# Optimization experiments

Hardware: AMD Instinct MI355X
Metric: run time of the kernel (lower is better)

The kernel has to match this reference:

```python
import jax, jax.numpy as jnp
import numpy as np

# Loss hyperparameters (from init_kwargs defaults)
ALPHA, BETA, GAMMA = 1.0, 2.0, 1.0
DAY_W, NIGHT_W = 2.0, 0.5
PEAK_WIN_W, PEAK_WIN = 3.0, 2
HIGH_POWER_W, POWER_PCT = 1.5, 0.75
HOURS = 24

B, S = 4096, 4032  # seq_len = 24 * 168 days


def setup_inputs() -> dict:
    key = jax.random.key(0)
    k1, k2 = jax.random.split(key)
    y_true = jax.random.uniform(k1, (B, S), dtype=jnp.float32)
    # predictions = truth + noise, clipped to be realistic power values
    y_pred = y_true + 0.1 * jax.random.normal(k2, (B, S), dtype=jnp.float32)
    return {"y_pred": y_pred, "y_true": y_true}


def _daily_peaks(y, day_mask):
    # y, day_mask: (B, D, H). Peaks restricted to daytime hours.
    masked = jnp.where(day_mask, y, jnp.float32(-1e9))
    times = jnp.argmax(masked, axis=-1)                                   # (B, D) int
    vals = jnp.take_along_axis(y, times[..., None], axis=-1)[..., 0]      # (B, D)
    return times, vals


def reference(y_pred, y_true):
    b, s = y_true.shape
    d = s // HOURS
    # default is_daytime: hour-of-day in [6, 20]
    hour = jnp.arange(HOURS, dtype=jnp.int32)
    day_hour_mask = (hour >= 6) & (hour <= 20)                            # (H,)
    is_daytime = jnp.broadcast_to(day_hour_mask[None, None, :], (b, d, HOURS))

    yt = y_true.reshape(b, d, HOURS)
    yp = y_pred.reshape(b, d, HOURS)

    true_times, true_peaks = _daily_peaks(yt, is_daytime)
    pred_times, pred_peaks = _daily_peaks(yp, is_daytime)
    peak_time_errors = (pred_times - true_times).astype(jnp.float32)      # (B, D)

    # --- step weights: day/night base, x PEAK_WIN_W in [peak-2, peak+2] ---
    base_w = jnp.where(is_daytime, jnp.float32(DAY_W), jnp.float32(NIGHT_W))  # (B,D,H)
    pt = true_times[..., None]                                            # (B,D,1)
    in_window = (hour[None, None, :] >= pt - PEAK_WIN) & (hour[None, None, :] <= pt + PEAK_WIN)
    step_w = base_w * jnp.where(in_window, jnp.float32(PEAK_WIN_W), jnp.float32(1.0))
    step_w = step_w.reshape(b, s)

    sq_err = (y_pred - y_true) ** 2
    L_overall = jnp.sum(sq_err * step_w) / jnp.sum(step_w)

    # --- peak magnitude loss with high-power sample weighting ---
    sample_avg_peaks = jnp.mean(true_peaks, axis=1)                       # (B,)
    thr = jnp.quantile(sample_avg_peaks, POWER_PCT)
    high = sample_avg_peaks > thr                                         # (B,) bool
    sample_w = jnp.where(high[:, None], jnp.float32(HIGH_POWER_W), jnp.float32(1.0))
    sample_w = jnp.broadcast_to(sample_w, true_peaks.shape)               # (B, D)
    peak_sq = (pred_peaks - true_peaks) ** 2
    L_peak_mag = jnp.sum(peak_sq * sample_w) / jnp.sum(sample_w)

    L_peak_timing = jnp.mean(jnp.abs(peak_time_errors) * 10.0)

    return ALPHA * L_overall + BETA * L_peak_mag + GAMMA * L_peak_timing
```

## Files before the change

### kernel.cpp

```cpp
#include <hip/hip_runtime.h>
#include <math.h>

#define HOURS   24
#define DPS     168
#define S_LEN   4032
#define SPB     3
#define NB_MAX  4096


__global__ __launch_bounds__(512) void day_kernel(
    const float* __restrict__ yTrue, const float* __restrict__ yPred,
    float* __restrict__ A, float* __restrict__ P,
    float* __restrict__ SEb, float* __restrict__ SWb, float* __restrict__ Tb,
    int nB)
{
    __shared__ float s_a[SPB * DPS + 8];
    __shared__ float s_p[SPB * DPS + 8];
    __shared__ float s_red[3][8];

    const int tid = threadIdx.x;
    const int lane = tid & 63;
    const int wv = tid >> 6;

    const int s  = tid / DPS;
    const int ds = tid - s * DPS;
    const int b  = blockIdx.x * SPB + s;
    const bool valid = (tid < SPB * DPS) && (b < nB);

    const long long d = valid ? ((long long)b * DPS + ds) : 0;

    const float4* gt = (const float4*)(yTrue + d * HOURS);
    const float4* gp = (const float4*)(yPred + d * HOURS);

    float4 t0 = gt[0], t1 = gt[1], t2 = gt[2], t3 = gt[3], t4 = gt[4], t5 = gt[5];
    float4 p0 = gp[0], p1 = gp[1], p2 = gp[2], p3 = gp[3], p4 = gp[4], p5 = gp[5];

    float yt[24], yp[24];
    yt[0]=t0.x; yt[1]=t0.y; yt[2]=t0.z; yt[3]=t0.w;
    yt[4]=t1.x; yt[5]=t1.y; yt[6]=t1.z; yt[7]=t1.w;
    yt[8]=t2.x; yt[9]=t2.y; yt[10]=t2.z; yt[11]=t2.w;
    yt[12]=t3.x; yt[13]=t3.y; yt[14]=t3.z; yt[15]=t3.w;
    yt[16]=t4.x; yt[17]=t4.y; yt[18]=t4.z; yt[19]=t4.w;
    yt[20]=t5.x; yt[21]=t5.y; yt[22]=t5.z; yt[23]=t5.w;
    yp[0]=p0.x; yp[1]=p0.y; yp[2]=p0.z; yp[3]=p0.w;
    yp[4]=p1.x; yp[5]=p1.y; yp[6]=p1.z; yp[7]=p1.w;
    yp[8]=p2.x; yp[9]=p2.y; yp[10]=p2.z; yp[11]=p2.w;
    yp[12]=p3.x; yp[13]=p3.y; yp[14]=p3.z; yp[15]=p3.w;
    yp[16]=p4.x; yp[17]=p4.y; yp[18]=p4.z; yp[19]=p4.w;
    yp[20]=p5.x; yp[21]=p5.y; yp[22]=p5.z; yp[23]=p5.w;

    float tbest = yt[6]; int tt = 6;
#pragma unroll
    for (int h = 7; h <= 20; ++h) if (yt[h] > tbest) { tbest = yt[h]; tt = h; }
    float pbest = yp[6]; int pt = 6;
#pragma unroll
    for (int h = 7; h <= 20; ++h) if (yp[h] > pbest) { pbest = yp[h]; pt = h; }

    float se = 0.f, sw = 0.f;
#pragma unroll
    for (int h = 0; h < 24; ++h) {
        float bw = ((h >= 6) && (h <= 20)) ? 2.0f : 0.5f;
        float wgt = bw * (((h >= tt - 2) && (h <= tt + 2)) ? 3.0f : 1.0f);
        float dd = yp[h] - yt[h];
        se = fmaf(wgt * dd, dd, se);
        sw += wgt;
    }
    float te = fabsf((float)(pt - tt));
    if (!valid) { se = 0.f; sw = 0.f; te = 0.f; }

    if (tid < SPB * DPS) {
        float dpk = pbest - tbest;
        s_a[tid] = valid ? tbest : 0.f;
        s_p[tid] = valid ? dpk * dpk : 0.f;
    }

#pragma unroll
    for (int o = 32; o > 0; o >>= 1) {
        se += __shfl_down(se, o, 64);
        sw += __shfl_down(sw, o, 64);
        te += __shfl_down(te, o, 64);
    }
    if (lane == 0) { s_red[0][wv] = se; s_red[1][wv] = sw; s_red[2][wv] = te; }
    __syncthreads();

    if (tid == 0) {
        float e = 0.f, w = 0.f, t = 0.f;
#pragma unroll
        for (int k = 0; k < 8; ++k) { e += s_red[0][k]; w += s_red[1][k]; t += s_red[2][k]; }
        SEb[blockIdx.x] = e; SWb[blockIdx.x] = w; Tb[blockIdx.x] = t;
    }

    if (wv < SPB) {
        const int bb = blockIdx.x * SPB + wv;
        const float* sa = s_a + wv * DPS;
        const float* sp = s_p + wv * DPS;
        float a = sa[lane] + sa[lane + 64];
        float p = sp[lane] + sp[lane + 64];
        if (lane < DPS - 128) { a += sa[lane + 128]; p += sp[lane + 128]; }
#pragma unroll
        for (int o = 32; o > 0; o >>= 1) {
            a += __shfl_down(a, o, 64);
            p += __shfl_down(p, o, 64);
        }
        if (lane == 0 && bb < nB) {
            A[bb] = a * (1.0f / (float)DPS);
            P[bb] = p;
        }
    }
}


__global__ __launch_bounds__(256) void rank_kernel(
    const float* __restrict__ A, float* __restrict__ qout, int nB)
{
    __shared__ float sA[NB_MAX];
    const int tid = threadIdx.x;

    for (int i = tid; i < nB; i += 256) sA[i] = A[i];
    __syncthreads();

    const int b = blockIdx.x * 64 + (tid >> 2);
    const int quar = tid & 3;
    if (b >= nB) return;
    const float v = sA[b];
    const int span = nB / 4;
    const float4* s4 = (const float4*)(sA + quar * span);

    int cl = 0, ce = 0;
    for (int i = 0; i < span / 4; ++i) {
        float4 x = s4[i];
        cl += (x.x < v) + (x.y < v) + (x.z < v) + (x.w < v);
        ce += (x.x == v) + (x.y == v) + (x.z == v) + (x.w == v);
    }
    cl += __shfl_xor(cl, 1, 64); ce += __shfl_xor(ce, 1, 64);
    cl += __shfl_xor(cl, 2, 64); ce += __shfl_xor(ce, 2, 64);

    if (quar == 0) {
        double pos = 0.75 * (double)(nB - 1);
        int lo = (int)pos;
        int hi = (lo + 1 < nB) ? lo + 1 : lo;
        if (lo >= cl && lo < cl + ce) qout[0] = v;
        if (hi >= cl && hi < cl + ce) qout[1] = v;
    }
}


__device__ inline double block_reduce_d(double v, double* scratch, int tid) {
#pragma unroll
    for (int o = 32; o > 0; o >>= 1) v += __shfl_down(v, o, 64);
    if ((tid & 63) == 0) scratch[tid >> 6] = v;
    __syncthreads();
    double r = 0.0;
    if (tid == 0) r = scratch[0] + scratch[1] + scratch[2] + scratch[3];
    __syncthreads();
    return r;
}

__global__ __launch_bounds__(256) void final_kernel(
    const float* __restrict__ SEb, const float* __restrict__ SWb,
    const float* __restrict__ Tb, const float* __restrict__ P,
    const float* __restrict__ A, const float* __restrict__ qout,
    float* __restrict__ out, int nB, int nBlk)
{
    __shared__ double s_dred[4];
    const int tid = threadIdx.x;

    double pos = 0.75 * (double)(nB - 1);
    double frac = pos - (double)((int)pos);
    float thr = (float)((double)qout[0] + frac * ((double)qout[1] - (double)qout[0]));

    double se = 0.0, sw = 0.0, te = 0.0, wp = 0.0, wsum = 0.0;
    for (int i = tid; i < nBlk; i += 256) {
        se += (double)SEb[i];
        sw += (double)SWb[i];
        te += (double)Tb[i];
    }
    for (int b = tid; b < nB; b += 256) {
        float w = (A[b] > thr) ? 1.5f : 1.0f;
        wp   += (double)w * (double)P[b];
        wsum += (double)w;
    }
    se   = block_reduce_d(se,   s_dred, tid);
    sw   = block_reduce_d(sw,   s_dred, tid);
    te   = block_reduce_d(te,   s_dred, tid);
    wp   = block_reduce_d(wp,   s_dred, tid);
    wsum = block_reduce_d(wsum, s_dred, tid);

    if (tid == 0) {
        double L_overall = se / sw;
        double L_peak    = wp / ((double)DPS * wsum);
        double L_timing  = 10.0 * te / ((double)nB * (double)DPS);
        out[0] = (float)(L_overall + 2.0 * L_peak + L_timing);
    }
}


extern "C" void kernel_launch(void* const* d_in, const int* in_sizes, int n_in,
                              void* d_out, int out_size, void* d_ws, size_t ws_size,
                              hipStream_t stream) {
    const float* y_pred = (const float*)d_in[0];
    const float* y_true = (const float*)d_in[1];
    int total = in_sizes[0];
    int nB = total / S_LEN;
    int nBlk = (nB + SPB - 1) / SPB;

    float* ws  = (float*)d_ws;
    float* A   = ws;
    float* P   = A   + (size_t)nB;
    float* SEb = P   + (size_t)nB;
    float* SWb = SEb + (size_t)nBlk;
    float* Tb  = SWb + (size_t)nBlk;
    float* q   = Tb  + (size_t)nBlk;

    day_kernel<<<nBlk, 512, 0, stream>>>(y_true, y_pred, A, P, SEb, SWb, Tb, nB);
    rank_kernel<<<(nB + 63) / 64, 256, 0, stream>>>(A, q, nB);
    final_kernel<<<1, 256, 0, stream>>>(SEb, SWb, Tb, P, A, q, (float*)d_out, nB, nBlk);
}
```

Measured before the change: 164.5 us.

## Split each day across six threads with coalesced float4 loads per sample block

```diff
diff --git a/kernel.cpp b/kernel.cpp
--- a/kernel.cpp
+++ b/kernel.cpp
@@ -4,108 +4,133 @@
 #define HOURS   24
 #define DPS     168
 #define S_LEN   4032
-#define SPB     3
 #define NB_MAX  4096
-
-
-__global__ __launch_bounds__(512) void day_kernel(
+#define NEG     -1e9f
+
+
+__global__ __launch_bounds__(1024, 8) void day_kernel(
     const float* __restrict__ yTrue, const float* __restrict__ yPred,
     float* __restrict__ A, float* __restrict__ P,
     float* __restrict__ SEb, float* __restrict__ SWb, float* __restrict__ Tb,
     int nB)
 {
-    __shared__ float s_a[SPB * DPS + 8];
-    __shared__ float s_p[SPB * DPS + 8];
-    __shared__ float s_red[3][8];
-
-    const int tid = threadIdx.x;
+    __shared__ float s_val[1024];
+    __shared__ int   s_idx[1024];
+    __shared__ int   s_tt[DPS];
+    __shared__ float s_red[16];
+    __shared__ float s_samp[3][4];
+
+    const int tid  = threadIdx.x;
     const int lane = tid & 63;
-    const int wv = tid >> 6;
-
-    const int s  = tid / DPS;
-    const int ds = tid - s * DPS;
-    const int b  = blockIdx.x * SPB + s;
-    const bool valid = (tid < SPB * DPS) && (b < nB);
-
-    const long long d = valid ? ((long long)b * DPS + ds) : 0;
-
-    const float4* gt = (const float4*)(yTrue + d * HOURS);
-    const float4* gp = (const float4*)(yPred + d * HOURS);
-
-    float4 t0 = gt[0], t1 = gt[1], t2 = gt[2], t3 = gt[3], t4 = gt[4], t5 = gt[5];
-    float4 p0 = gp[0], p1 = gp[1], p2 = gp[2], p3 = gp[3], p4 = gp[4], p5 = gp[5];
-
-    float yt[24], yp[24];
-    yt[0]=t0.x; yt[1]=t0.y; yt[2]=t0.z; yt[3]=t0.w;
-    yt[4]=t1.x; yt[5]=t1.y; yt[6]=t1.z; yt[7]=t1.w;
-    yt[8]=t2.x; yt[9]=t2.y; yt[10]=t2.z; yt[11]=t2.w;
-    yt[12]=t3.x; yt[13]=t3.y; yt[14]=t3.z; yt[15]=t3.w;
-    yt[16]=t4.x; yt[17]=t4.y; yt[18]=t4.z; yt[19]=t4.w;
-    yt[20]=t5.x; yt[21]=t5.y; yt[22]=t5.z; yt[23]=t5.w;
-    yp[0]=p0.x; yp[1]=p0.y; yp[2]=p0.z; yp[3]=p0.w;
-    yp[4]=p1.x; yp[5]=p1.y; yp[6]=p1.z; yp[7]=p1.w;
-    yp[8]=p2.x; yp[9]=p2.y; yp[10]=p2.z; yp[11]=p2.w;
-    yp[12]=p3.x; yp[13]=p3.y; yp[14]=p3.z; yp[15]=p3.w;
-    yp[16]=p4.x; yp[17]=p4.y; yp[18]=p4.z; yp[19]=p4.w;
-    yp[20]=p5.x; yp[21]=p5.y; yp[22]=p5.z; yp[23]=p5.w;
-
-    float tbest = yt[6]; int tt = 6;
-#pragma unroll
-    for (int h = 7; h <= 20; ++h) if (yt[h] > tbest) { tbest = yt[h]; tt = h; }
-    float pbest = yp[6]; int pt = 6;
-#pragma unroll
-    for (int h = 7; h <= 20; ++h) if (yp[h] > pbest) { pbest = yp[h]; pt = h; }
-
-    float se = 0.f, sw = 0.f;
-#pragma unroll
-    for (int h = 0; h < 24; ++h) {
-        float bw = ((h >= 6) && (h <= 20)) ? 2.0f : 0.5f;
-        float wgt = bw * (((h >= tt - 2) && (h <= tt + 2)) ? 3.0f : 1.0f);
-        float dd = yp[h] - yt[h];
-        se = fmaf(wgt * dd, dd, se);
-        sw += wgt;
-    }
-    float te = fabsf((float)(pt - tt));
-    if (!valid) { se = 0.f; sw = 0.f; te = 0.f; }
-
-    if (tid < SPB * DPS) {
-        float dpk = pbest - tbest;
-        s_a[tid] = valid ? tbest : 0.f;
-        s_p[tid] = valid ? dpk * dpk : 0.f;
-    }
-
-#pragma unroll
-    for (int o = 32; o > 0; o >>= 1) {
-        se += __shfl_down(se, o, 64);
-        sw += __shfl_down(sw, o, 64);
-        te += __shfl_down(te, o, 64);
-    }
-    if (lane == 0) { s_red[0][wv] = se; s_red[1][wv] = sw; s_red[2][wv] = te; }
+    const int wv   = tid >> 6;
+    const int b    = blockIdx.x;
+    const bool valid = (tid < DPS * 6);
+
+    const int li  = valid ? tid : 0;
+    const int day = li / 6;
+    const int q   = li - day * 6;
+    const int h0  = q << 2;
+
+    const float4* gt = (const float4*)(yTrue + (size_t)b * S_LEN);
+    const float4* gp = (const float4*)(yPred + (size_t)b * S_LEN);
+    const float4 t = gt[li];
+    const float4 p = gp[li];
+
+    const bool m0 = (q >= 2);
+    const bool m1 = (q >= 2) && (q <= 4);
+    const bool m2 = (q >= 1) && (q <= 4);
+    const bool m3 = m2;
+
+    float bv = NEG; int bh = h0;
+    { float v;
+      v = m0 ? t.x : NEG; if (v > bv) { bv = v; bh = h0;     }
+      v = m1 ? t.y : NEG; if (v > bv) { bv = v; bh = h0 + 1; }
+      v = m2 ? t.z : NEG; if (v > bv) { bv = v; bh = h0 + 2; }
+      v = m3 ? t.w : NEG; if (v > bv) { bv = v; bh = h0 + 3; } }
+    s_val[tid] = bv; s_idx[tid] = bh;
+    __syncthreads();
+
+    int tt = 0; float tb = 0.f;
+    if (tid < DPS) {
+        const int base = tid * 6;
+        float v = s_val[base]; int hb = s_idx[base];
+#pragma unroll
+        for (int j = 1; j < 6; ++j) {
+            const float vj = s_val[base + j]; const int hj = s_idx[base + j];
+            if (vj > v) { v = vj; hb = hj; }
+        }
+        tt = hb; tb = v;
+        s_tt[tid] = hb;
+    }
+    __syncthreads();
+
+    const int ttd = s_tt[day];
+    float bpv = NEG; int bph = h0;
+    { float v;
+      v = m0 ? p.x : NEG; if (v > bpv) { bpv = v; bph = h0;     }
+      v = m1 ? p.y : NEG; if (v > bpv) { bpv = v; bph = h0 + 1; }
+      v = m2 ? p.z : NEG; if (v > bpv) { bpv = v; bph = h0 + 2; }
+      v = m3 ? p.w : NEG; if (v > bpv) { bpv = v; bph = h0 + 3; } }
+
+    const int wlo = ttd - 2, whi = ttd + 2;
+    float se = 0.f;
+    { float bw, w, d; int h;
+      h = h0;     bw = m0 ? 2.f : 0.5f; w = (h >= wlo && h <= whi) ? 3.f * bw : bw; d = p.x - t.x; se = fmaf(w * d, d, se);
+      h = h0 + 1; bw = m1 ? 2.f : 0.5f; w = (h >= wlo && h <= whi) ? 3.f * bw : bw; d = p.y - t.y; se = fmaf(w * d, d, se);
+      h = h0 + 2; bw = m2 ? 2.f : 0.5f; w = (h >= wlo && h <= whi) ? 3.f * bw : bw; d = p.z - t.z; se = fmaf(w * d, d, se);
+      h = h0 + 3; bw = m3 ? 2.f : 0.5f; w = (h >= wlo && h <= whi) ? 3.f * bw : bw; d = p.w - t.w; se = fmaf(w * d, d, se); }
+    if (!valid) se = 0.f;
+    s_val[tid] = bpv; s_idx[tid] = bph;
+
+#pragma unroll
+    for (int o = 32; o > 0; o >>= 1) se += __shfl_down(se, o, 64);
+    if (lane == 0) s_red[wv] = se;
+    __syncthreads();
+
+    if (tid < 192) {
+        float tbv = 0.f, dpk2 = 0.f, sw = 0.f, te = 0.f;
+        if (tid < DPS) {
+            const int base = tid * 6;
+            float v = s_val[base]; int hb = s_idx[base];
+#pragma unroll
+            for (int j = 1; j < 6; ++j) {
+                const float vj = s_val[base + j]; const int hj = s_idx[base + j];
+                if (vj > v) { v = vj; hb = hj; }
+            }
+            const int n = max(0, 8 - tt) + max(0, tt - 18);
+            sw = 54.5f - 3.f * (float)n;
+            te = fabsf((float)(hb - tt));
+            const float dpk = v - tb;
+            dpk2 = dpk * dpk;
+            tbv = tb;
+        }
+#pragma unroll
+        for (int o = 32; o > 0; o >>= 1) {
+            tbv  += __shfl_down(tbv,  o, 64);
+            dpk2 += __shfl_down(dpk2, o, 64);
+            sw   += __shfl_down(sw,   o, 64);
+            te   += __shfl_down(te,   o, 64);
+        }
+        if (lane == 0) {
+            s_samp[wv][0] = tbv; s_samp[wv][1] = dpk2;
+            s_samp[wv][2] = sw;  s_samp[wv][3] = te;
+        }
+    }
     __syncthreads();
 
     if (tid == 0) {
-        float e = 0.f, w = 0.f, t = 0.f;
-#pragma unroll
-        for (int k = 0; k < 8; ++k) { e += s_red[0][k]; w += s_red[1][k]; t += s_red[2][k]; }
-        SEb[blockIdx.x] = e; SWb[blockIdx.x] = w; Tb[blockIdx.x] = t;
-    }
-
-    if (wv < SPB) {
-        const int bb = blockIdx.x * SPB + wv;
-        const float* sa = s_a + wv * DPS;
-        const float* sp = s_p + wv * DPS;
-        float a = sa[lane] + sa[lane + 64];
-        float p = sp[lane] + sp[lane + 64];
-        if (lane < DPS - 128) { a += sa[lane + 128]; p += sp[lane + 128]; }
-#pragma unroll
-        for (int o = 32; o > 0; o >>= 1) {
-            a += __shfl_down(a, o, 64);
-            p += __shfl_down(p, o, 64);
-        }
-        if (lane == 0 && bb < nB) {
-            A[bb] = a * (1.0f / (float)DPS);
-            P[bb] = p;
-        }
+        const float sA = s_samp[0][0] + s_samp[1][0] + s_samp[2][0];
+        const float sP = s_samp[0][1] + s_samp[1][1] + s_samp[2][1];
+        const float sW = s_samp[0][2] + s_samp[1][2] + s_samp[2][2];
+        const float sT = s_samp[0][3] + s_samp[1][3] + s_samp[2][3];
+        float e = 0.f;
+#pragma unroll
+        for (int k = 0; k < 16; ++k) e += s_red[k];
+        A[b]   = sA * (1.0f / (float)DPS);
+        P[b]   = sP;
+        SEb[b] = e;
+        SWb[b] = sW;
+        Tb[b]  = sT;
     }
 }
 
@@ -202,17 +227,16 @@
     const float* y_true = (const float*)d_in[1];
     int total = in_sizes[0];
     int nB = total / S_LEN;
-    int nBlk = (nB + SPB - 1) / SPB;
 
     float* ws  = (float*)d_ws;
     float* A   = ws;
     float* P   = A   + (size_t)nB;
     float* SEb = P   + (size_t)nB;
-    float* SWb = SEb + (size_t)nBlk;
-    float* Tb  = SWb + (size_t)nBlk;
-    float* q   = Tb  + (size_t)nBlk;
-
-    day_kernel<<<nBlk, 512, 0, stream>>>(y_true, y_pred, A, P, SEb, SWb, Tb, nB);
+    float* SWb = SEb + (size_t)nB;
+    float* Tb  = SWb + (size_t)nB;
+    float* q   = Tb  + (size_t)nB;
+
+    day_kernel<<<nB, 1024, 0, stream>>>(y_true, y_pred, A, P, SEb, SWb, Tb, nB);
     rank_kernel<<<(nB + 63) / 64, 256, 0, stream>>>(A, q, nB);
-    final_kernel<<<1, 256, 0, stream>>>(SEb, SWb, Tb, P, A, q, (float*)d_out, nB, nBlk);
-}
+    final_kernel<<<1, 256, 0, stream>>>(SEb, SWb, Tb, P, A, q, (float*)d_out, nB, nB);
+}
```

Result: no change. 162.4 us (-1.3%).

## Map one wavefront per sample with 8 lanes per day for coalesced loads

Applied to the files above, without the earlier changes.

```diff
diff --git a/kernel.cpp b/kernel.cpp
--- a/kernel.cpp
+++ b/kernel.cpp
@@ -4,108 +4,101 @@
 #define HOURS   24
 #define DPS     168
 #define S_LEN   4032
-#define SPB     3
 #define NB_MAX  4096
-
-
-__global__ __launch_bounds__(512) void day_kernel(
+#define NEG     -1e9f
+
+struct F3 { float x, y, z; };
+
+
+__global__ __launch_bounds__(256) void day_kernel(
     const float* __restrict__ yTrue, const float* __restrict__ yPred,
     float* __restrict__ A, float* __restrict__ P,
     float* __restrict__ SEb, float* __restrict__ SWb, float* __restrict__ Tb,
     int nB)
 {
-    __shared__ float s_a[SPB * DPS + 8];
-    __shared__ float s_p[SPB * DPS + 8];
-    __shared__ float s_red[3][8];
-
-    const int tid = threadIdx.x;
+    const int tid  = threadIdx.x;
     const int lane = tid & 63;
-    const int wv = tid >> 6;
-
-    const int s  = tid / DPS;
-    const int ds = tid - s * DPS;
-    const int b  = blockIdx.x * SPB + s;
-    const bool valid = (tid < SPB * DPS) && (b < nB);
-
-    const long long d = valid ? ((long long)b * DPS + ds) : 0;
-
-    const float4* gt = (const float4*)(yTrue + d * HOURS);
-    const float4* gp = (const float4*)(yPred + d * HOURS);
-
-    float4 t0 = gt[0], t1 = gt[1], t2 = gt[2], t3 = gt[3], t4 = gt[4], t5 = gt[5];
-    float4 p0 = gp[0], p1 = gp[1], p2 = gp[2], p3 = gp[3], p4 = gp[4], p5 = gp[5];
-
-    float yt[24], yp[24];
-    yt[0]=t0.x; yt[1]=t0.y; yt[2]=t0.z; yt[3]=t0.w;
-    yt[4]=t1.x; yt[5]=t1.y; yt[6]=t1.z; yt[7]=t1.w;
-    yt[8]=t2.x; yt[9]=t2.y; yt[10]=t2.z; yt[11]=t2.w;
-    yt[12]=t3.x; yt[13]=t3.y; yt[14]=t3.z; yt[15]=t3.w;
-    yt[16]=t4.x; yt[17]=t4.y; yt[18]=t4.z; yt[19]=t4.w;
-    yt[20]=t5.x; yt[21]=t5.y; yt[22]=t5.z; yt[23]=t5.w;
-    yp[0]=p0.x; yp[1]=p0.y; yp[2]=p0.z; yp[3]=p0.w;
-    yp[4]=p1.x; yp[5]=p1.y; yp[6]=p1.z; yp[7]=p1.w;
-    yp[8]=p2.x; yp[9]=p2.y; yp[10]=p2.z; yp[11]=p2.w;
-    yp[12]=p3.x; yp[13]=p3.y; yp[14]=p3.z; yp[15]=p3.w;
-    yp[16]=p4.x; yp[17]=p4.y; yp[18]=p4.z; yp[19]=p4.w;
-    yp[20]=p5.x; yp[21]=p5.y; yp[22]=p5.z; yp[23]=p5.w;
-
-    float tbest = yt[6]; int tt = 6;
-#pragma unroll
-    for (int h = 7; h <= 20; ++h) if (yt[h] > tbest) { tbest = yt[h]; tt = h; }
-    float pbest = yp[6]; int pt = 6;
-#pragma unroll
-    for (int h = 7; h <= 20; ++h) if (yp[h] > pbest) { pbest = yp[h]; pt = h; }
-
-    float se = 0.f, sw = 0.f;
-#pragma unroll
-    for (int h = 0; h < 24; ++h) {
-        float bw = ((h >= 6) && (h <= 20)) ? 2.0f : 0.5f;
-        float wgt = bw * (((h >= tt - 2) && (h <= tt + 2)) ? 3.0f : 1.0f);
-        float dd = yp[h] - yt[h];
-        se = fmaf(wgt * dd, dd, se);
-        sw += wgt;
-    }
-    float te = fabsf((float)(pt - tt));
-    if (!valid) { se = 0.f; sw = 0.f; te = 0.f; }
-
-    if (tid < SPB * DPS) {
-        float dpk = pbest - tbest;
-        s_a[tid] = valid ? tbest : 0.f;
-        s_p[tid] = valid ? dpk * dpk : 0.f;
+    const int wv   = tid >> 6;
+    const int b    = blockIdx.x * 4 + wv;
+    if (b >= nB) return;
+
+    const int j  = lane & 7;
+    const int h0 = 3 * j;
+
+    const bool m0 = (h0     >= 6) && (h0     <= 20);
+    const bool m1 = (h0 + 1 >= 6) && (h0 + 1 <= 20);
+    const bool m2 = (h0 + 2 >= 6) && (h0 + 2 <= 20);
+    const float bw0 = m0 ? 2.f : 0.5f;
+    const float bw1 = m1 ? 2.f : 0.5f;
+    const float bw2 = m2 ? 2.f : 0.5f;
+
+    const F3* gt = (const F3*)(yTrue + (size_t)b * S_LEN);
+    const F3* gp = (const F3*)(yPred + (size_t)b * S_LEN);
+
+    F3 tq[3], pq[3];
+    tq[0] = gt[lane];       pq[0] = gp[lane];
+    tq[1] = gt[64 + lane];  pq[1] = gp[64 + lane];
+
+    float se = 0.f, ts = 0.f, dp = 0.f, sww = 0.f, te = 0.f;
+
+#pragma unroll
+    for (int it = 0; it < 21; ++it) {
+        if (it + 2 < 21) {
+            tq[(it + 2) % 3] = gt[(it + 2) * 64 + lane];
+            pq[(it + 2) % 3] = gp[(it + 2) * 64 + lane];
+        }
+        const F3 t = tq[it % 3];
+        const F3 p = pq[it % 3];
+
+        float bv = m0 ? t.x : NEG; int bh = h0;
+        { float v;
+          v = m1 ? t.y : NEG; if (v > bv) { bv = v; bh = h0 + 1; }
+          v = m2 ? t.z : NEG; if (v > bv) { bv = v; bh = h0 + 2; } }
+        float qv = m0 ? p.x : NEG; int qh = h0;
+        { float v;
+          v = m1 ? p.y : NEG; if (v > qv) { qv = v; qh = h0 + 1; }
+          v = m2 ? p.z : NEG; if (v > qv) { qv = v; qh = h0 + 2; } }
+
+#pragma unroll
+        for (int o = 1; o <= 4; o <<= 1) {
+            float ov = __shfl_xor(bv, o, 64);
+            int   oh = __shfl_xor(bh, o, 64);
+            if (ov > bv || (ov == bv && oh < bh)) { bv = ov; bh = oh; }
+            float pv = __shfl_xor(qv, o, 64);
+            int   ph = __shfl_xor(qh, o, 64);
+            if (pv > qv || (pv == qv && ph < qh)) { qv = pv; qh = ph; }
+        }
+        const float tb = bv; const int tt = bh;
+        const float pb = qv; const int pt = qh;
+
+        const int wlo = tt - 2, whi = tt + 2;
+        { float d, w;
+          d = p.x - t.x; w = ((h0     >= wlo) && (h0     <= whi)) ? 3.f * bw0 : bw0; se = fmaf(w * d, d, se);
+          d = p.y - t.y; w = ((h0 + 1 >= wlo) && (h0 + 1 <= whi)) ? 3.f * bw1 : bw1; se = fmaf(w * d, d, se);
+          d = p.z - t.z; w = ((h0 + 2 >= wlo) && (h0 + 2 <= whi)) ? 3.f * bw2 : bw2; se = fmaf(w * d, d, se); }
+
+        ts += tb;
+        const float dpk = pb - tb;
+        dp = fmaf(dpk, dpk, dp);
+        const int n = max(0, 8 - tt) + max(0, tt - 18);
+        sww += 54.5f - 3.f * (float)n;
+        te += fabsf((float)(pt - tt));
     }
 
 #pragma unroll
     for (int o = 32; o > 0; o >>= 1) {
-        se += __shfl_down(se, o, 64);
-        sw += __shfl_down(sw, o, 64);
-        te += __shfl_down(te, o, 64);
-    }
-    if (lane == 0) { s_red[0][wv] = se; s_red[1][wv] = sw; s_red[2][wv] = te; }
-    __syncthreads();
-
-    if (tid == 0) {
-        float e = 0.f, w = 0.f, t = 0.f;
-#pragma unroll
-        for (int k = 0; k < 8; ++k) { e += s_red[0][k]; w += s_red[1][k]; t += s_red[2][k]; }
-        SEb[blockIdx.x] = e; SWb[blockIdx.x] = w; Tb[blockIdx.x] = t;
-    }
-
-    if (wv < SPB) {
-        const int bb = blockIdx.x * SPB + wv;
-        const float* sa = s_a + wv * DPS;
-        const float* sp = s_p + wv * DPS;
-        float a = sa[lane] + sa[lane + 64];
-        float p = sp[lane] + sp[lane + 64];
-        if (lane < DPS - 128) { a += sa[lane + 128]; p += sp[lane + 128]; }
-#pragma unroll
-        for (int o = 32; o > 0; o >>= 1) {
-            a += __shfl_down(a, o, 64);
-            p += __shfl_down(p, o, 64);
-        }
-        if (lane == 0 && bb < nB) {
-            A[bb] = a * (1.0f / (float)DPS);
-            P[bb] = p;
-        }
+        se  += __shfl_down(se,  o, 64);
+        ts  += __shfl_down(ts,  o, 64);
+        dp  += __shfl_down(dp,  o, 64);
+        sww += __shfl_down(sww, o, 64);
+        te  += __shfl_down(te,  o, 64);
+    }
+    if (lane == 0) {
+        A[b]   = ts * 0.125f * (1.0f / (float)DPS);
+        P[b]   = dp * 0.125f;
+        SEb[b] = se;
+        SWb[b] = sww * 0.125f;
+        Tb[b]  = te * 0.125f;
     }
 }
 
@@ -202,17 +195,16 @@
     const float* y_true = (const float*)d_in[1];
     int total = in_sizes[0];
     int nB = total / S_LEN;
-    int nBlk = (nB + SPB - 1) / SPB;
 
     float* ws  = (float*)d_ws;
     float* A   = ws;
     float* P   = A   + (size_t)nB;
     float* SEb = P   + (size_t)nB;
-    float* SWb = SEb + (size_t)nBlk;
-    float* Tb  = SWb + (size_t)nBlk;
-    float* q   = Tb  + (size_t)nBlk;
-
-    day_kernel<<<nBlk, 512, 0, stream>>>(y_true, y_pred, A, P, SEb, SWb, Tb, nB);
+    float* SWb = SEb + (size_t)nB;
+    float* Tb  = SWb + (size_t)nB;
+    float* q   = Tb  + (size_t)nB;
+
+    day_kernel<<<(nB + 3) / 4, 256, 0, stream>>>(y_true, y_pred, A, P, SEb, SWb, Tb, nB);
     rank_kernel<<<(nB + 63) / 64, 256, 0, stream>>>(A, q, nB);
-    final_kernel<<<1, 256, 0, stream>>>(SEb, SWb, Tb, P, A, q, (float*)d_out, nB, nBlk);
-}
+    final_kernel<<<1, 256, 0, stream>>>(SEb, SWb, Tb, P, A, q, (float*)d_out, nB, nB);
+}
```

After: 173.6 us. 1.05x slower.
